# Optimization experiments

Hardware: AMD Instinct MI355X
Metric: run time of the kernel (lower is better)

The kernel has to match this reference:

```python
import jax, jax.numpy as jnp
import numpy as np

N = 100000
E = 1600000
IN_DIM, H1, H2 = 64, 128, 64


def gcn_conv(x, edge_index, W, b, n_nodes):
    """PyG-style GCNConv: add self-loops, symmetric normalization, x@W, scatter-add, +bias."""
    src, dst = edge_index[0], edge_index[1]
    loop = jnp.arange(n_nodes)
    src = jnp.concatenate([src, loop])
    dst = jnp.concatenate([dst, loop])
    deg = jax.ops.segment_sum(jnp.ones_like(src, dtype=x.dtype), dst, num_segments=n_nodes)
    dinv = jax.lax.rsqrt(deg)  # deg >= 1 due to self loops
    norm = dinv[src] * dinv[dst]  # [E+N]
    xw = x @ W  # [N, out] - transform before gather (out <= in keeps traffic low)
    msg = xw[src] * norm[:, None]  # [E+N, out]
    out = jax.ops.segment_sum(msg, dst, num_segments=n_nodes)
    return out + b


def setup_inputs() -> dict:
    key = jax.random.key(0)
    ks = jax.random.split(key, 8)
    x = jax.random.normal(ks[0], (N, IN_DIM), dtype=jnp.float32)
    edge_index = jax.random.randint(ks[1], (2, E), 0, N, dtype=jnp.int64)
    W1 = jax.random.normal(ks[2], (IN_DIM, H1), dtype=jnp.float32) / np.sqrt(IN_DIM)
    b1 = jnp.zeros((H1,), dtype=jnp.float32)
    W2 = jax.random.normal(ks[3], (H1, H2), dtype=jnp.float32) / np.sqrt(H1)
    b2 = jnp.zeros((H2,), dtype=jnp.float32)
    Wfc = jax.random.normal(ks[4], (H2, 1), dtype=jnp.float32) / np.sqrt(H2)
    bfc = jnp.zeros((1,), dtype=jnp.float32)
    return {"x": x, "edge_index": edge_index, "W1": W1, "b1": b1,
            "W2": W2, "b2": b2, "Wfc": Wfc, "bfc": bfc}


def reference(x, edge_index, W1, b1, W2, b2, Wfc, bfc):
    h = jax.nn.relu(gcn_conv(x, edge_index, W1, b1, N))
    h = jax.nn.relu(gcn_conv(h, edge_index, W2, b2, N))
    return (h @ Wfc + bfc).reshape(-1)  # [N]
```

## Files before the change

### kernel.cpp

```cpp
#include <hip/hip_runtime.h>


constexpr int NN = 100000;
constexpr int NE = 1600000;
constexpr int D0 = 64;
constexpr int D1 = 128;
constexpr int D2 = 64;
constexpr int NB = (NN + 255) / 256;
constexpr int TILE = 8192;
constexpr int NT = (NE + TILE - 1) / TILE;
constexpr int H1STRIDE = 132;
constexpr int NH = NN / 2;

typedef unsigned short u16;
typedef unsigned int u32;
typedef __attribute__((ext_vector_type(8))) short short8;
typedef __attribute__((ext_vector_type(4))) float f32x4;
typedef _Float16 h4 __attribute__((ext_vector_type(4)));


__device__ __forceinline__ float4 scale4(const float4& a, float s) {
    return float4{a.x * s, a.y * s, a.z * s, a.w * s};
}

__device__ __forceinline__ void addh8(float4& a, float4& b, uint4 u) {
    h4 h0 = *(h4*)&u.x;
    h4 h1 = *(h4*)&u.z;
    a.x += (float)h0[0]; a.y += (float)h0[1]; a.z += (float)h0[2]; a.w += (float)h0[3];
    b.x += (float)h1[0]; b.y += (float)h1[1]; b.z += (float)h1[2]; b.w += (float)h1[3];
}

__device__ __forceinline__ uint2 packh4(const float4& v) {
    h4 h;
    h[0] = (_Float16)v.x; h[1] = (_Float16)v.y;
    h[2] = (_Float16)v.z; h[3] = (_Float16)v.w;
    return *(uint2*)&h;
}

__device__ __forceinline__ void xor_reduce8(float4& a, float4& b, int mask) {
    a.x += __shfl_xor(a.x, mask, 64);
    a.y += __shfl_xor(a.y, mask, 64);
    a.z += __shfl_xor(a.z, mask, 64);
    a.w += __shfl_xor(a.w, mask, 64);
    b.x += __shfl_xor(b.x, mask, 64);
    b.y += __shfl_xor(b.y, mask, 64);
    b.z += __shfl_xor(b.z, mask, 64);
    b.w += __shfl_xor(b.w, mask, 64);
}

__device__ __forceinline__ u16 f2bf(float f) {
    u32 u = __float_as_uint(f);
    return (u16)((u + 0x7fffu + ((u >> 16) & 1u)) >> 16);
}
__device__ __forceinline__ float bf2f(u16 h) {
    return __uint_as_float(((u32)h) << 16);
}

__global__ __launch_bounds__(256) void k_splitW(const float* __restrict__ W1,
                                                const float* __restrict__ W2,
                                                u16* __restrict__ W1h, u16* __restrict__ W1l,
                                                u16* __restrict__ W2h, u16* __restrict__ W2l,
                                                int* __restrict__ gbcnt) {
    if (blockIdx.x == 32) {
        int t = threadIdx.x;
        gbcnt[t] = 0;
        gbcnt[t + 256] = 0;
        return;
    }
    int i = blockIdx.x * 256 + threadIdx.x;
    int j = i & 7;
    int l = (i >> 3) & 63;
    int ts = i >> 9;
    int kf = ((l >> 4) << 3) + j;
    int cl = l & 15;
    {
        int s = ts >> 3, t = ts & 7;
        float w = W1[(s * 32 + kf) * D1 + t * 16 + cl];
        u16 h = f2bf(w);
        W1h[i] = h;
        W1l[i] = f2bf(w - bf2f(h));
    }
    {
        int s = ts >> 2, t = ts & 3;
        float w = W2[(s * 32 + kf) * D2 + t * 16 + cl];
        u16 h = f2bf(w);
        W2h[i] = h;
        W2l[i] = f2bf(w - bf2f(h));
    }
}

__global__ __launch_bounds__(256) void k_bcount(const int* __restrict__ dst,
                                                int* __restrict__ gbcnt,
                                                int* __restrict__ tcnt) {
    __shared__ int cnt_s[NB];
    int tid = threadIdx.x;
    int e0 = blockIdx.x * TILE;
    int ecnt = NE - e0 < TILE ? NE - e0 : TILE;
    for (int i = tid; i < NB; i += 256) cnt_s[i] = 0;
    __syncthreads();
    for (int i = tid; i < ecnt; i += 256)
        atomicAdd(&cnt_s[dst[e0 + i] >> 8], 1);
    __syncthreads();
    int* trow = tcnt + (size_t)blockIdx.x * NB;
    for (int i = tid; i < NB; i += 256) {
        int c = cnt_s[i];
        trow[i] = c;
        if (c) atomicAdd(&gbcnt[i], c);
    }
}

__global__ __launch_bounds__(512) void k_scan_bsum(const int* __restrict__ gbcnt,
                                                   int* __restrict__ bsum,
                                                   int* __restrict__ gcur) {
    __shared__ int s[512];
    int tid = threadIdx.x;
    int v = (tid < NB) ? gbcnt[tid] : 0;
    s[tid] = v;
    __syncthreads();
#pragma unroll
    for (int off = 1; off < 512; off <<= 1) {
        int t = (tid >= off) ? s[tid - off] : 0;
        __syncthreads();
        s[tid] += t;
        __syncthreads();
    }
    int ex = s[tid] - v;
    if (tid <= NB) bsum[tid] = ex;
    if (tid < NB) gcur[tid] = ex;
}

__global__ __launch_bounds__(256) void k_part(const int* __restrict__ src,
                                              const int* __restrict__ dst,
                                              const int* __restrict__ tcnt,
                                              int* __restrict__ gcur,
                                              unsigned* __restrict__ packed) {
    __shared__ int gbase_s[NB];
    __shared__ int cur_s[NB];
    int tid = threadIdx.x;
    int e0 = blockIdx.x * TILE;
    int ecnt = NE - e0 < TILE ? NE - e0 : TILE;
    const int* trow = tcnt + (size_t)blockIdx.x * NB;
    for (int i = tid; i < NB; i += 256) {
        int c = trow[i];
        gbase_s[i] = c ? atomicAdd(&gcur[i], c) : 0;
        cur_s[i] = 0;
    }
    __syncthreads();
    for (int i = tid; i < ecnt; i += 256) {
        int d = dst[e0 + i];
        int s = src[e0 + i];
        int b = d >> 8;
        int slot = atomicAdd(&cur_s[b], 1);
        packed[gbase_s[b] + slot] = ((unsigned)(d & 255) << 24) | (unsigned)s;
    }
}

__global__ __launch_bounds__(256) void k_bucket(const int* __restrict__ bsum,
                                                const unsigned* __restrict__ packed,
                                                const float* __restrict__ x,
                                                int* __restrict__ rowptr,
                                                float* __restrict__ dinv,
                                                int* __restrict__ col,
                                                u16* __restrict__ xs) {
    __shared__ int hist[256];
    __shared__ int s[256];
    __shared__ int cur[256];
    __shared__ float dinv_s[256];
    int b = blockIdx.x;
    int tid = threadIdx.x;
    int e0 = bsum[b], e1 = bsum[b + 1];
    hist[tid] = 0;
    __syncthreads();
    for (int e = e0 + tid; e < e1; e += 256)
        atomicAdd(&hist[packed[e] >> 24], 1);
    __syncthreads();
    int v = hist[tid];
    int n = (b << 8) + tid;
    float di = rsqrtf((float)(v + 1));
    dinv_s[tid] = di;
    if (n < NN) dinv[n] = di;
    s[tid] = v;
    __syncthreads();
#pragma unroll
    for (int off = 1; off < 256; off <<= 1) {
        int t = (tid >= off) ? s[tid - off] : 0;
        __syncthreads();
        s[tid] += t;
        __syncthreads();
    }
    int base = e0 + s[tid] - v;
    if (n <= NN) rowptr[n] = base;
    cur[tid] = base;
    __syncthreads();
    for (int e = e0 + tid; e < e1; e += 256) {
        unsigned p = packed[e];
        int pos = atomicAdd(&cur[p >> 24], 1);
        col[pos] = (int)((p & 0xFFFFFFu) << 5);
    }
    int n_hi = NN - (b << 8);
    if (n_hi > 256) n_hi = 256;
    for (int i = tid; i < n_hi * 16; i += 256) {
        int nl = i >> 4;
        int k4 = i & 15;
        int q = k4 >> 2;
        int nn = (b << 8) + nl;
        uint2 w = packh4(scale4(((const float4*)x)[(size_t)nn * 16 + k4], dinv_s[nl]));
        ((uint2*)xs)[((size_t)q * NN + nn) * 4 + (k4 & 3)] = w;
    }
}

__global__ __launch_bounds__(256) void k_gather1s(const int* __restrict__ rowptr,
                                                  const int* __restrict__ colb,
                                                  const u16* __restrict__ xs,
                                                  const float* __restrict__ dinv,
                                                  float* __restrict__ agg) {
    int bid = blockIdx.x;
    int sh = bid & 7;
    int s = sh >> 1, h = sh & 1;
    int tid = threadIdx.x;
    int lane = tid & 63;
    int wv = tid >> 6;
    int n = h * NH + (bid >> 3) * 32 + wv * 8 + (lane >> 3);
    if (n >= (h + 1) * NH) return;
    int half = lane & 1;
    int es = (lane >> 1) & 3;
    int r0 = rowptr[n], r1 = rowptr[n + 1];
    const char* base = (const char*)xs + (size_t)s * NN * 32 + half * 16;
    float4 a{0, 0, 0, 0}, b{0, 0, 0, 0};
    if (es == 0) addh8(a, b, *(const uint4*)(base + (size_t)n * 32));
    int e = r0 + es;
    for (; e + 4 < r1; e += 8) {
        int c0 = colb[e];
        int c1 = colb[e + 4];
        uint4 v0 = *(const uint4*)(base + c0);
        uint4 v1 = *(const uint4*)(base + c1);
        addh8(a, b, v0);
        addh8(a, b, v1);
    }
    for (; e < r1; e += 4)
        addh8(a, b, *(const uint4*)(base + colb[e]));
    xor_reduce8(a, b, 2);
    xor_reduce8(a, b, 4);
    if (es == 0) {
        float di = dinv[n];
        float* ag = agg + ((size_t)s * NN + n) * 16 + half * 8;
        *(float4*)ag = scale4(a, di);
        *(float4*)(ag + 4) = scale4(b, di);
    }
}

__global__ __launch_bounds__(256) void k_gemm12(const float* __restrict__ agg,
                                                const u16* __restrict__ W1h,
                                                const u16* __restrict__ W1l,
                                                const float* __restrict__ b1,
                                                const u16* __restrict__ W2h,
                                                const u16* __restrict__ W2l,
                                                const float* __restrict__ dinv,
                                                u16* __restrict__ y2) {
    __shared__ u32 h1s[64 * H1STRIDE];
    int tid = threadIdx.x;
    int l = tid & 63;
    int wv = tid >> 6;
    int n_base = blockIdx.x * 64;
    int row_a = l & 15;
    int kg = (l >> 4) << 3;
    int crow = (l >> 4) * 4;

    short8 Ah[2], Al[2];
#pragma unroll
    for (int s = 0; s < 2; ++s) {
        int an = n_base + wv * 16 + row_a;
        if (an >= NN) an = NN - 1;
        int q = (s * 32 + kg) >> 4;
        int off = kg & 8;
        const float* ap = agg + ((size_t)q * NN + an) * 16 + off;
        f32x4 v0 = *(const f32x4*)ap;
        f32x4 v1 = *(const f32x4*)(ap + 4);
#pragma unroll
        for (int j = 0; j < 4; ++j) {
            u16 h0 = f2bf(v0[j]);
            Ah[s][j] = (short)h0;
            Al[s][j] = (short)f2bf(v0[j] - bf2f(h0));
            u16 h1b = f2bf(v1[j]);
            Ah[s][j + 4] = (short)h1b;
            Al[s][j + 4] = (short)f2bf(v1[j] - bf2f(h1b));
        }
    }
#pragma unroll
    for (int t = 0; t < 8; ++t) {
        f32x4 acc = {0.f, 0.f, 0.f, 0.f};
#pragma unroll
        for (int s = 0; s < 2; ++s) {
            short8 Bh = *(const short8*)(W1h + ((size_t)(s * 8 + t) * 64 + l) * 8);
            short8 Bl = *(const short8*)(W1l + ((size_t)(s * 8 + t) * 64 + l) * 8);
            acc = __builtin_amdgcn_mfma_f32_16x16x32_bf16(Ah[s], Bh, acc, 0, 0, 0);
            acc = __builtin_amdgcn_mfma_f32_16x16x32_bf16(Ah[s], Bl, acc, 0, 0, 0);
            acc = __builtin_amdgcn_mfma_f32_16x16x32_bf16(Al[s], Bh, acc, 0, 0, 0);
        }
        float bb = b1[t * 16 + (l & 15)];
        int kcol = t * 16 + (l & 15);
#pragma unroll
        for (int r = 0; r < 4; ++r) {
            int row = wv * 16 + crow + r;
            float v = fmaxf(acc[r] + bb, 0.f);
            u16 h = f2bf(v);
            u16 lo = f2bf(v - bf2f(h));
            h1s[row * H1STRIDE + kcol] = (u32)h | ((u32)lo << 16);
        }
    }
    __syncthreads();

    short8 A2h[4], A2l[4];
#pragma unroll
    for (int s = 0; s < 4; ++s) {
        int row = wv * 16 + row_a;
        const u32* hp = &h1s[row * H1STRIDE + s * 32 + kg];
        uint4 p0 = *(const uint4*)hp;
        uint4 p1 = *(const uint4*)(hp + 4);
        u32 pv[8] = {p0.x, p0.y, p0.z, p0.w, p1.x, p1.y, p1.z, p1.w};
#pragma unroll
        for (int j = 0; j < 8; ++j) {
            A2h[s][j] = (short)(pv[j] & 0xffffu);
            A2l[s][j] = (short)(pv[j] >> 16);
        }
    }
#pragma unroll
    for (int t = 0; t < 4; ++t) {
        f32x4 acc = {0.f, 0.f, 0.f, 0.f};
#pragma unroll
        for (int s = 0; s < 4; ++s) {
            short8 Bh = *(const short8*)(W2h + ((size_t)(s * 4 + t) * 64 + l) * 8);
            short8 Bl = *(const short8*)(W2l + ((size_t)(s * 4 + t) * 64 + l) * 8);
            acc = __builtin_amdgcn_mfma_f32_16x16x32_bf16(A2h[s], Bh, acc, 0, 0, 0);
            acc = __builtin_amdgcn_mfma_f32_16x16x32_bf16(A2h[s], Bl, acc, 0, 0, 0);
            acc = __builtin_amdgcn_mfma_f32_16x16x32_bf16(A2l[s], Bh, acc, 0, 0, 0);
        }
#pragma unroll
        for (int r = 0; r < 4; ++r) {
            int n = n_base + wv * 16 + crow + r;
            if (n < NN) {
                _Float16 hf = (_Float16)(acc[r] * dinv[n]);
                y2[((size_t)t * NN + n) * 16 + (l & 15)] = *(u16*)&hf;
            }
        }
    }
}

__global__ __launch_bounds__(256) void k_gather2s(const int* __restrict__ rowptr,
                                                  const int* __restrict__ colb,
                                                  const u16* __restrict__ y2,
                                                  const float* __restrict__ dinv,
                                                  const float* __restrict__ b2,
                                                  const float* __restrict__ Wfc,
                                                  float* __restrict__ partial) {
    int bid = blockIdx.x;
    int sh = bid & 7;
    int s = sh >> 1, h = sh & 1;
    int tid = threadIdx.x;
    int lane = tid & 63;
    int wv = tid >> 6;
    int n = h * NH + (bid >> 3) * 32 + wv * 8 + (lane >> 3);
    if (n >= (h + 1) * NH) return;
    int half = lane & 1;
    int es = (lane >> 1) & 3;
    int r0 = rowptr[n], r1 = rowptr[n + 1];
    const char* base = (const char*)y2 + (size_t)s * NN * 32 + half * 16;
    float4 a{0, 0, 0, 0}, b{0, 0, 0, 0};
    if (es == 0) addh8(a, b, *(const uint4*)(base + (size_t)n * 32));
    int e = r0 + es;
    for (; e + 4 < r1; e += 8) {
        int c0 = colb[e];
        int c1 = colb[e + 4];
        uint4 v0 = *(const uint4*)(base + c0);
        uint4 v1 = *(const uint4*)(base + c1);
        addh8(a, b, v0);
        addh8(a, b, v1);
    }
    for (; e < r1; e += 4)
        addh8(a, b, *(const uint4*)(base + colb[e]));
    xor_reduce8(a, b, 2);
    xor_reduce8(a, b, 4);
    float di = dinv[n];
    int fo = s * 16 + half * 8;
    float4 b0 = *(const float4*)(b2 + fo);
    float4 b1v = *(const float4*)(b2 + fo + 4);
    float4 w0 = *(const float4*)(Wfc + fo);
    float4 w1 = *(const float4*)(Wfc + fo + 4);
    float p = fmaxf(fmaf(a.x, di, b0.x), 0.f) * w0.x
            + fmaxf(fmaf(a.y, di, b0.y), 0.f) * w0.y
            + fmaxf(fmaf(a.z, di, b0.z), 0.f) * w0.z
            + fmaxf(fmaf(a.w, di, b0.w), 0.f) * w0.w
            + fmaxf(fmaf(b.x, di, b1v.x), 0.f) * w1.x
            + fmaxf(fmaf(b.y, di, b1v.y), 0.f) * w1.y
            + fmaxf(fmaf(b.z, di, b1v.z), 0.f) * w1.z
            + fmaxf(fmaf(b.w, di, b1v.w), 0.f) * w1.w;
    p += __shfl_xor(p, 1, 64);
    if ((lane & 7) == 0 && es == 0) partial[(size_t)s * NN + n] = p;
}

__global__ __launch_bounds__(256) void k_head(const float* __restrict__ partial,
                                              const float* __restrict__ bfc,
                                              float* __restrict__ out) {
    int i = blockIdx.x * 256 + threadIdx.x;
    if (i >= NN) return;
    out[i] = partial[i] + partial[NN + i] + partial[2 * NN + i]
           + partial[3 * NN + i] + bfc[0];
}

extern "C" void kernel_launch(void* const* d_in, const int* in_sizes, int n_in,
                              void* d_out, int out_size, void* d_ws, size_t ws_size,
                              hipStream_t stream) {
    const float* x   = (const float*)d_in[0];
    const int*   ei  = (const int*)d_in[1];
    const float* W1  = (const float*)d_in[2];
    const float* b1  = (const float*)d_in[3];
    const float* W2  = (const float*)d_in[4];
    const float* b2  = (const float*)d_in[5];
    const float* Wfc = (const float*)d_in[6];
    const float* bfc = (const float*)d_in[7];
    float* out = (float*)d_out;

    const int* src = ei;
    const int* dst = ei + NE;

    char* ws = (char*)d_ws;
    size_t o = 0;
    auto alloc = [&](size_t bytes) { char* p = ws + o; o += (bytes + 255) & ~size_t(255); return p; };
    int*   scratch = (int*)alloc(NN * 4);
    int*   rowptr = (int*)alloc((NN + 1) * 4);
    int*   bsum   = (int*)alloc(512 * 4);
    int*   gcur   = (int*)alloc(NB * 4);
    float* dinv   = (float*)alloc(NN * 4);
    int*   col    = (int*)alloc((size_t)NE * 4);
    u16*   xs     = (u16*)alloc((size_t)NN * D0 * 2);
    float* agg1x  = (float*)alloc((size_t)NN * D0 * 4);
    u16*   y2     = (u16*)alloc((size_t)NN * D2 * 2);
    float* partial= (float*)alloc((size_t)NN * 4 * 4);
    unsigned* packed = (unsigned*)agg1x;
    int* gbcnt = scratch;
    u16* W1h = (u16*)(scratch + 512);
    u16* W1l = W1h + 8192;
    u16* W2h = W1l + 8192;
    u16* W2l = W2h + 8192;
    int* tcnt = scratch + 512 + 16384;

    const int GB = 8 * ((NH + 31) / 32);

    k_splitW    <<<33, 256, 0, stream>>>(W1, W2, W1h, W1l, W2h, W2l, gbcnt);
    k_bcount    <<<NT, 256, 0, stream>>>(dst, gbcnt, tcnt);
    k_scan_bsum <<<1, 512, 0, stream>>>(gbcnt, bsum, gcur);
    k_part      <<<NT, 256, 0, stream>>>(src, dst, tcnt, gcur, packed);
    k_bucket    <<<NB, 256, 0, stream>>>(bsum, packed, x, rowptr, dinv, col, xs);

    k_gather1s  <<<GB, 256, 0, stream>>>(rowptr, col, xs, dinv, agg1x);
    k_gemm12    <<<(NN + 63) / 64, 256, 0, stream>>>(agg1x, W1h, W1l, b1, W2h, W2l, dinv, y2);
    k_gather2s  <<<GB, 256, 0, stream>>>(rowptr, col, y2, dinv, b2, Wfc, partial);
    k_head      <<<(NN + 255) / 256, 256, 0, stream>>>(partial, bfc, out);
}
```

Measured before the change: 249.5 us.

## Sort nodes by degree into a permutation to balance gather wavefronts

Builds a degree histogram in the bucket kernel, scans it, and computes a node permutation grouped by in-degree (capped at 63). Both gather kernels then walk nodes through this permutation, so the eight nodes sharing a wavefront have similar edge counts and lanes idle less on divergent loop lengths. The cost is two extra small kernel launches, global atomics, and one more indirection per node. Nodes in a block are no longer contiguous, which may hurt locality of the rowptr, dinv and output accesses.

```diff
diff --git a/kernel.cpp b/kernel.cpp
--- a/kernel.cpp
+++ b/kernel.cpp
@@ -60,11 +60,13 @@
                                                 const float* __restrict__ W2,
                                                 u16* __restrict__ W1h, u16* __restrict__ W1l,
                                                 u16* __restrict__ W2h, u16* __restrict__ W2l,
-                                                int* __restrict__ gbcnt) {
+                                                int* __restrict__ gbcnt,
+                                                int* __restrict__ gdeg) {
     if (blockIdx.x == 32) {
         int t = threadIdx.x;
         gbcnt[t] = 0;
         gbcnt[t + 256] = 0;
+        if (t < 64) gdeg[t] = 0;
         return;
     }
     int i = blockIdx.x * 256 + threadIdx.x;
@@ -161,15 +163,18 @@
                                                 int* __restrict__ rowptr,
                                                 float* __restrict__ dinv,
                                                 int* __restrict__ col,
-                                                u16* __restrict__ xs) {
+                                                u16* __restrict__ xs,
+                                                int* __restrict__ gdeg) {
     __shared__ int hist[256];
     __shared__ int s[256];
     __shared__ int cur[256];
     __shared__ float dinv_s[256];
+    __shared__ int dh[64];
     int b = blockIdx.x;
     int tid = threadIdx.x;
     int e0 = bsum[b], e1 = bsum[b + 1];
     hist[tid] = 0;
+    if (tid < 64) dh[tid] = 0;
     __syncthreads();
     for (int e = e0 + tid; e < e1; e += 256)
         atomicAdd(&hist[packed[e] >> 24], 1);
@@ -178,7 +183,10 @@
     int n = (b << 8) + tid;
     float di = rsqrtf((float)(v + 1));
     dinv_s[tid] = di;
-    if (n < NN) dinv[n] = di;
+    if (n < NN) {
+        dinv[n] = di;
+        atomicAdd(&dh[v > 63 ? 63 : v], 1);
+    }
     s[tid] = v;
     __syncthreads();
 #pragma unroll
@@ -188,6 +196,7 @@
         s[tid] += t;
         __syncthreads();
     }
+    if (tid < 64 && dh[tid]) atomicAdd(&gdeg[tid], dh[tid]);
     int base = e0 + s[tid] - v;
     if (n <= NN) rowptr[n] = base;
     cur[tid] = base;
@@ -209,8 +218,44 @@
     }
 }
 
+__global__ __launch_bounds__(64) void k_scan_deg(const int* __restrict__ gdeg,
+                                                 int* __restrict__ dcur) {
+    int tid = threadIdx.x;
+    int v = gdeg[tid];
+    int sum = v;
+#pragma unroll
+    for (int off = 1; off < 64; off <<= 1) {
+        int t = __shfl_up(sum, off, 64);
+        if (tid >= off) sum += t;
+    }
+    dcur[tid] = sum - v;
+}
+
+__global__ __launch_bounds__(256) void k_perm(const int* __restrict__ rowptr,
+                                              int* __restrict__ dcur,
+                                              int* __restrict__ perm) {
+    __shared__ int dh[64];
+    __shared__ int dbase[64];
+    int tid = threadIdx.x;
+    int n = blockIdx.x * 256 + tid;
+    if (tid < 64) dh[tid] = 0;
+    __syncthreads();
+    int bin = 0, slot = 0;
+    bool valid = n < NN;
+    if (valid) {
+        int d = rowptr[n + 1] - rowptr[n];
+        bin = d > 63 ? 63 : d;
+        slot = atomicAdd(&dh[bin], 1);
+    }
+    __syncthreads();
+    if (tid < 64) dbase[tid] = dh[tid] ? atomicAdd(&dcur[tid], dh[tid]) : 0;
+    __syncthreads();
+    if (valid) perm[dbase[bin] + slot] = n;
+}
+
 __global__ __launch_bounds__(256) void k_gather1s(const int* __restrict__ rowptr,
                                                   const int* __restrict__ colb,
+                                                  const int* __restrict__ perm,
                                                   const u16* __restrict__ xs,
                                                   const float* __restrict__ dinv,
                                                   float* __restrict__ agg) {
@@ -220,8 +265,9 @@
     int tid = threadIdx.x;
     int lane = tid & 63;
     int wv = tid >> 6;
-    int n = h * NH + (bid >> 3) * 32 + wv * 8 + (lane >> 3);
-    if (n >= (h + 1) * NH) return;
+    int idx = h * NH + (bid >> 3) * 32 + wv * 8 + (lane >> 3);
+    if (idx >= (h + 1) * NH) return;
+    int n = perm[idx];
     int half = lane & 1;
     int es = (lane >> 1) & 3;
     int r0 = rowptr[n], r1 = rowptr[n + 1];
@@ -348,6 +394,7 @@
 
 __global__ __launch_bounds__(256) void k_gather2s(const int* __restrict__ rowptr,
                                                   const int* __restrict__ colb,
+                                                  const int* __restrict__ perm,
                                                   const u16* __restrict__ y2,
                                                   const float* __restrict__ dinv,
                                                   const float* __restrict__ b2,
@@ -359,8 +406,9 @@
     int tid = threadIdx.x;
     int lane = tid & 63;
     int wv = tid >> 6;
-    int n = h * NH + (bid >> 3) * 32 + wv * 8 + (lane >> 3);
-    if (n >= (h + 1) * NH) return;
+    int idx = h * NH + (bid >> 3) * 32 + wv * 8 + (lane >> 3);
+    if (idx >= (h + 1) * NH) return;
+    int n = perm[idx];
     int half = lane & 1;
     int es = (lane >> 1) & 3;
     int r0 = rowptr[n], r1 = rowptr[n + 1];
@@ -432,6 +480,7 @@
     int*   gcur   = (int*)alloc(NB * 4);
     float* dinv   = (float*)alloc(NN * 4);
     int*   col    = (int*)alloc((size_t)NE * 4);
+    int*   perm   = (int*)alloc(NN * 4);
     u16*   xs     = (u16*)alloc((size_t)NN * D0 * 2);
     float* agg1x  = (float*)alloc((size_t)NN * D0 * 4);
     u16*   y2     = (u16*)alloc((size_t)NN * D2 * 2);
@@ -443,17 +492,21 @@
     u16* W2h = W1l + 8192;
     u16* W2l = W2h + 8192;
     int* tcnt = scratch + 512 + 16384;
+    int* gdeg = tcnt + (size_t)NT * NB;
+    int* dcur = gdeg + 64;
 
     const int GB = 8 * ((NH + 31) / 32);
 
-    k_splitW    <<<33, 256, 0, stream>>>(W1, W2, W1h, W1l, W2h, W2l, gbcnt);
+    k_splitW    <<<33, 256, 0, stream>>>(W1, W2, W1h, W1l, W2h, W2l, gbcnt, gdeg);
     k_bcount    <<<NT, 256, 0, stream>>>(dst, gbcnt, tcnt);
     k_scan_bsum <<<1, 512, 0, stream>>>(gbcnt, bsum, gcur);
     k_part      <<<NT, 256, 0, stream>>>(src, dst, tcnt, gcur, packed);
-    k_bucket    <<<NB, 256, 0, stream>>>(bsum, packed, x, rowptr, dinv, col, xs);
-
-    k_gather1s  <<<GB, 256, 0, stream>>>(rowptr, col, xs, dinv, agg1x);
+    k_bucket    <<<NB, 256, 0, stream>>>(bsum, packed, x, rowptr, dinv, col, xs, gdeg);
+    k_scan_deg  <<<1, 64, 0, stream>>>(gdeg, dcur);
+    k_perm      <<<NB, 256, 0, stream>>>(rowptr, dcur, perm);
+
+    k_gather1s  <<<GB, 256, 0, stream>>>(rowptr, col, perm, xs, dinv, agg1x);
     k_gemm12    <<<(NN + 63) / 64, 256, 0, stream>>>(agg1x, W1h, W1l, b1, W2h, W2l, dinv, y2);
-    k_gather2s  <<<GB, 256, 0, stream>>>(rowptr, col, y2, dinv, b2, Wfc, partial);
+    k_gather2s  <<<GB, 256, 0, stream>>>(rowptr, col, perm, y2, dinv, b2, Wfc, partial);
     k_head      <<<(NN + 255) / 256, 256, 0, stream>>>(partial, bfc, out);
 }
```

Measured after the change: 294.0 us. 17.9% more time.
